# Kernel tuning notes

Measured on AMD Instinct MI355X. Metric: run time of the kernel, lower is better.

Reference implementation:

```python
import jax, jax.numpy as jnp
import numpy as np

NEG_INF = -1e30

def dwconv1(x, dw, db, pw, pb):
    # DWConv with kernel_size=1: depthwise = per-channel scale+bias, pointwise = dense linear.
    # x: [B, L, H]
    return (x * dw + db) @ pw.T + pb

def masked_softmax(logits, maskf, axis):
    # masked_softmax as in SQuAD repos: mask*logits + (1-mask)*(-1e30), then softmax over axis
    m = maskf * logits + (1.0 - maskf) * NEG_INF
    return jax.nn.softmax(m, axis=axis)

def setup_inputs() -> dict:
    key = jax.random.key(0)
    ks = jax.random.split(key, 20)
    B, L, H = 4, 4096, 1024
    s = 1.0 / np.sqrt(H)
    inp = {
        "x": jax.random.normal(ks[0], (B, L, H), dtype=jnp.float32),
        "mask": jax.random.randint(ks[1], (B, L), 0, 2, dtype=jnp.int32),
    }
    names = ["k", "q", "v", "r"]
    for i, n in enumerate(names):
        inp[n + "_dw"] = jax.random.normal(ks[2 + 4 * i], (H,), dtype=jnp.float32) * 0.1 + 1.0
        inp[n + "_db"] = jnp.zeros((H,), dtype=jnp.float32)
        inp[n + "_pw"] = jax.random.normal(ks[3 + 4 * i], (H, H), dtype=jnp.float32) * s
        inp[n + "_pb"] = jnp.zeros((H,), dtype=jnp.float32)
    return inp

def reference(x, mask, k_dw, k_db, k_pw, k_pb, q_dw, q_db, q_pw, q_pb,
              v_dw, v_db, v_pw, v_pb, r_dw, r_db, r_pw, r_pb):
    B, L, H = x.shape
    n_head = 16
    hc = H // n_head
    maskf = mask.astype(x.dtype)[:, None, None, :]  # [B,1,1,L]

    def heads(t):  # [B,L,H] -> [B,nh,hc,L]
        return t.reshape(B, L, n_head, hc).transpose(0, 2, 3, 1)

    keys = heads(dwconv1(x, k_dw, k_db, k_pw, k_pb))
    queries = heads(dwconv1(x, q_dw, q_db, q_pw, q_pb))
    values = heads(dwconv1(x, v_dw, v_db, v_pw, v_pb))

    key_sm = masked_softmax(keys, maskf, axis=3)      # softmax over L
    query_sm = masked_softmax(queries, maskf, axis=2)  # softmax over head channels

    # context = key @ value^T : [B,nh,hc,hc]
    context = jnp.einsum("bhcl,bhdl->bhcd", key_sm, values)
    # attended = context^T @ query : [B,nh,hc(value),L]
    attended = jnp.einsum("bhcd,bhcl->bhdl", context, query_sm)

    agg = attended.transpose(0, 3, 1, 2).reshape(B, L, H)  # concat heads, [B,L,H]
    # dropout is identity in eval mode
    return dwconv1(agg, r_dw, r_db, r_pw, r_pb)
```

## Files before the change

### kernel.cpp

```cpp
#include <hip/hip_runtime.h>
#include <stdint.h>

#define H 1024
#define LSEQ 4096
#define NBATCH 4
#define MT (NBATCH*LSEQ)

typedef __attribute__((ext_vector_type(8))) short bf16x8;
typedef __attribute__((ext_vector_type(4))) short s16x4;
typedef __attribute__((ext_vector_type(4))) float f32x4;
typedef __attribute__((ext_vector_type(16))) float f32x16;

static __device__ __forceinline__ unsigned short f2bf(float f){
  union { float f; unsigned u; } v; v.f = f;
  unsigned u = v.u;
  return (unsigned short)((u + 0x7FFFu + ((u >> 16) & 1u)) >> 16);
}
static __device__ __forceinline__ float bf2f(unsigned short h){
  union { unsigned u; float f; } v; v.u = ((unsigned)h) << 16;
  return v.f;
}
static __device__ __forceinline__ void g2l16(const void* g, void* l){
  __builtin_amdgcn_global_load_lds((const __attribute__((address_space(1))) void*)g,
                                   (__attribute__((address_space(3))) void*)l, 16, 0, 0);
}
static __device__ __forceinline__ f32x4 mfma16(bf16x8 a, bf16x8 b, f32x4 c){
  return __builtin_amdgcn_mfma_f32_16x16x32_bf16(a, b, c, 0, 0, 0);
}
static __device__ __forceinline__ f32x16 mfma32(bf16x8 a, bf16x8 b, f32x16 c){
  return __builtin_amdgcn_mfma_f32_32x32x16_bf16(a, b, c, 0, 0, 0);
}

struct P4 { const float* pw[4]; const float* dw[4]; const float* db[4]; const float* pb[4]; };

__global__ __launch_bounds__(256) void prepcvt(P4 a, const float* __restrict__ x,
    short* __restrict__ wb, float* __restrict__ bo, short* __restrict__ xb){
  const int bid = blockIdx.x, t = threadIdx.x;
  if (bid < 4096){
    __shared__ float red[256];
    const int p = bid >> 10, j = bid & 1023;
    const float* row = a.pw[p] + (size_t)j * H;
    const float* dwp = a.dw[p];
    const float* dbp = a.db[p];
    float acc = 0.f;
    #pragma unroll
    for (int k = 0; k < 4; ++k){
      int i = k*256 + t;
      float pv = row[i];
      wb[((size_t)p*H + j)*H + i] = (short)f2bf(pv * dwp[i]);
      acc += dbp[i] * pv;
    }
    red[t] = acc; __syncthreads();
    for (int s = 128; s > 0; s >>= 1){
      if (t < s) red[t] += red[t+s];
      __syncthreads();
    }
    if (t == 0) bo[p*H + j] = a.pb[p][j] + red[0];
  } else {
    const size_t base = ((size_t)(bid - 4096) * 4096) + (size_t)t * 16;
    #pragma unroll
    for (int h2 = 0; h2 < 2; ++h2){
      const float4* p = (const float4*)(x + base + h2*8);
      float4 u = p[0], v = p[1];
      bf16x8 o;
      o[0]=(short)f2bf(u.x); o[1]=(short)f2bf(u.y); o[2]=(short)f2bf(u.z); o[3]=(short)f2bf(u.w);
      o[4]=(short)f2bf(v.x); o[5]=(short)f2bf(v.y); o[6]=(short)f2bf(v.z); o[7]=(short)f2bf(v.w);
      *(bf16x8*)(xb + base + h2*8) = o;
    }
  }
}

template<int MODE, int NBLK>
__global__ __launch_bounds__(512, 2) void gemm8(const short* __restrict__ A,
    const short* __restrict__ WBp, const float* __restrict__ bia,
    short* __restrict__ oq, short* __restrict__ okT, short* __restrict__ ovT,
    float* __restrict__ ofin){
  __shared__ __align__(16) short lsm[2][2][256*64];

  const int nwg = NBLK * 64;
  const int cpx = nwg >> 3;
  const int bid = blockIdx.x;
  const int swz = (bid & 7) * cpx + (bid >> 3);
  const int mb = swz / NBLK, nb = swz % NBLK;
  const int m0 = mb * 256, n0 = nb * 256;

  const int tid  = threadIdx.x;
  const int lane = tid & 63;
  const int w    = tid >> 6;
  const int wm   = w >> 2, wn = w & 3;
  const int l31 = lane & 31, l1 = lane >> 5;
  const int rl = lane >> 3, sl = lane & 7;
  const int srcsw = ((sl ^ rl) << 3);

#define STAGE_A(BUF_, Q_, KB_) \
  g2l16(A + (size_t)(m0 + (Q_)*64 + w*8 + rl)*H + (KB_) + srcsw, \
        &lsm[0][BUF_][((Q_)*64 + w*8)*64])
#define STAGE_B(BUF_, Q_, KB_) \
  g2l16(WBp + (size_t)(n0 + (Q_)*64 + w*8 + rl)*H + (KB_) + srcsw, \
        &lsm[1][BUF_][((Q_)*64 + w*8)*64])
#define RD_A(dst, BUF_, MF, S) { const int row_ = wm*128 + (MF)*32 + l31; \
  dst = *(const bf16x8*)&lsm[0][BUF_][row_*64 + ((((S)*2 + l1) ^ (row_&7))<<3)]; }
#define RD_B(dst, BUF_, NF, S) { const int row_ = wn*64 + (NF)*32 + l31; \
  dst = *(const bf16x8*)&lsm[1][BUF_][row_*64 + ((((S)*2 + l1) ^ (row_&7))<<3)]; }

  f32x16 acc[4][2] = {};
  bf16x8 aF[2][4], bF[2][4];

  STAGE_B(0,0,0); STAGE_B(0,1,0); STAGE_B(0,2,0); STAGE_B(0,3,0);
  STAGE_A(0,0,0); STAGE_A(0,2,0); STAGE_A(0,1,0); STAGE_A(0,3,0);
  asm volatile("s_waitcnt vmcnt(2)" ::: "memory");
  __builtin_amdgcn_s_barrier();

  #pragma unroll 2
  for (int t = 0; t < 16; ++t){
    const int buf = t & 1, sbuf = buf ^ 1;
    const int skb = ((t < 15) ? (t + 1) : 15) << 6;

    #pragma unroll
    for (int mf = 0; mf < 2; ++mf)
      #pragma unroll
      for (int s = 0; s < 4; ++s) RD_A(aF[mf][s], buf, mf, s);
    #pragma unroll
    for (int nf = 0; nf < 2; ++nf)
      #pragma unroll
      for (int s = 0; s < 4; ++s) RD_B(bF[nf][s], buf, nf, s);
    STAGE_B(sbuf, 0, skb); STAGE_B(sbuf, 1, skb);
    STAGE_B(sbuf, 2, skb); STAGE_B(sbuf, 3, skb);
    __builtin_amdgcn_s_setprio(1);
    #pragma unroll
    for (int s = 0; s < 4; ++s)
      #pragma unroll
      for (int mf = 0; mf < 2; ++mf)
        #pragma unroll
        for (int nf = 0; nf < 2; ++nf)
          acc[mf][nf] = mfma32(aF[mf][s], bF[nf][s], acc[mf][nf]);
    __builtin_amdgcn_s_setprio(0);
    asm volatile("s_waitcnt vmcnt(4)" ::: "memory");
    __builtin_amdgcn_s_barrier();

    #pragma unroll
    for (int mf = 0; mf < 2; ++mf)
      #pragma unroll
      for (int s = 0; s < 4; ++s) RD_A(aF[mf][s], buf, 2+mf, s);
    STAGE_A(sbuf, 0, skb); STAGE_A(sbuf, 2, skb);
    STAGE_A(sbuf, 1, skb); STAGE_A(sbuf, 3, skb);
    __builtin_amdgcn_s_setprio(1);
    #pragma unroll
    for (int s = 0; s < 4; ++s)
      #pragma unroll
      for (int mf = 0; mf < 2; ++mf)
        #pragma unroll
        for (int nf = 0; nf < 2; ++nf)
          acc[2+mf][nf] = mfma32(aF[mf][s], bF[nf][s], acc[2+mf][nf]);
    __builtin_amdgcn_s_setprio(0);
    asm volatile("s_waitcnt vmcnt(2)" ::: "memory");
    __builtin_amdgcn_s_barrier();
  }
#undef STAGE_A
#undef STAGE_B
#undef RD_A
#undef RD_B

  if (MODE == 1){
    #pragma unroll
    for (int nf = 0; nf < 2; ++nf){
      const int n = n0 + wn*64 + nf*32 + l31;
      const float bv = bia[n];
      #pragma unroll
      for (int mf = 0; mf < 4; ++mf)
        #pragma unroll
        for (int g = 0; g < 4; ++g){
          const int mbse = m0 + wm*128 + mf*32 + g*8 + 4*l1;
          #pragma unroll
          for (int j = 0; j < 4; ++j)
            ofin[(size_t)(mbse+j)*H + n] = acc[mf][nf][g*4+j] + bv;
        }
    }
  } else {
    const int p = n0 >> 10;
    if (p == 1){
      #pragma unroll
      for (int nf = 0; nf < 2; ++nf){
        const int n = n0 + wn*64 + nf*32 + l31;
        const float bv = bia[n];
        const int ch = n & 1023;
        #pragma unroll
        for (int mf = 0; mf < 4; ++mf)
          #pragma unroll
          for (int g = 0; g < 4; ++g){
            const int mbse = m0 + wm*128 + mf*32 + g*8 + 4*l1;
            #pragma unroll
            for (int j = 0; j < 4; ++j)
              oq[(size_t)(mbse+j)*H + ch] = (short)f2bf(acc[mf][nf][g*4+j] + bv);
          }
      }
    } else {
      asm volatile("s_waitcnt vmcnt(0)" ::: "memory");
      __syncthreads();
      char* sC = (char*)&lsm[0][0][0];
      #pragma unroll
      for (int nf = 0; nf < 2; ++nf){
        const int cr = wn*64 + nf*32 + l31;
        const float bv = bia[n0 + cr];
        #pragma unroll
        for (int mf = 0; mf < 4; ++mf)
          #pragma unroll
          for (int g = 0; g < 4; ++g){
            const int s8 = wm*32 + mf*8 + g*2 + l1;
            s16x4 v;
            #pragma unroll
            for (int j = 0; j < 4; ++j) v[j] = (short)f2bf(acc[mf][nf][g*4+j] + bv);
            *(s16x4*)(sC + cr*512 + ((s8 ^ ((cr & 7) << 1)) << 3)) = v;
          }
      }
      __syncthreads();
      short* ot = (p == 0) ? okT : ovT;
      const int ch0 = n0 & 1023, bb = m0 >> 12, lp0 = m0 & 4095;
      const int c = lane & 31;
      #pragma unroll
      for (int it = 0; it < 16; ++it){
        const int cr = it*16 + w*2 + (lane >> 5);
        bf16x8 vv = *(bf16x8*)(sC + cr*512 + ((c ^ (cr & 7)) << 4));
        *(bf16x8*)&ot[((size_t)bb*H + ch0 + cr)*LSEQ + lp0 + c*8] = vv;
      }
    }
  }
}

__global__ __launch_bounds__(256) void ctx_k(const short* __restrict__ kT,
    const short* __restrict__ vT, const int* __restrict__ mask,
    float* __restrict__ ctxP, float* __restrict__ mloc, float* __restrict__ dloc){
  const int lc = blockIdx.x, h = blockIdx.y, b = blockIdx.z;
  __shared__ __align__(16) short lK[64*64];
  __shared__ __align__(16) short lV[64*64];
  __shared__ float sMx[64];
  __shared__ float sDenP[4][64];
  __shared__ int sMk[64];
  const int tid = threadIdx.x, lane = tid & 63, w = tid >> 6;
  const short* kb = kT + (size_t)(b*16 + h)*64*LSEQ;
  const short* vb = vT + (size_t)(b*16 + h)*64*LSEQ;
  const int l0 = lc*1024;

  int mk16[16];
  {
    const int* mp = mask + (size_t)b*LSEQ + l0;
    int4 a0 = *(const int4*)&mp[lane*8];
    int4 a1 = *(const int4*)&mp[lane*8+4];
    int4 a2 = *(const int4*)&mp[512 + lane*8];
    int4 a3 = *(const int4*)&mp[512 + lane*8+4];
    mk16[0]=a0.x; mk16[1]=a0.y; mk16[2]=a0.z; mk16[3]=a0.w;
    mk16[4]=a1.x; mk16[5]=a1.y; mk16[6]=a1.z; mk16[7]=a1.w;
    mk16[8]=a2.x; mk16[9]=a2.y; mk16[10]=a2.z; mk16[11]=a2.w;
    mk16[12]=a3.x; mk16[13]=a3.y; mk16[14]=a3.z; mk16[15]=a3.w;
  }
  for (int c2 = 0; c2 < 16; ++c2){
    const int ch = w*16 + c2;
    const short* rp = kb + (size_t)ch*LSEQ + l0;
    bf16x8 v0 = *(const bf16x8*)&rp[lane*8];
    bf16x8 v1 = *(const bf16x8*)&rp[512 + lane*8];
    float mm = -1e30f;
    #pragma unroll
    for (int e = 0; e < 8; ++e) if (mk16[e])   mm = fmaxf(mm, bf2f((unsigned short)v0[e]));
    #pragma unroll
    for (int e = 0; e < 8; ++e) if (mk16[8+e]) mm = fmaxf(mm, bf2f((unsigned short)v1[e]));
    #pragma unroll
    for (int off = 32; off >= 1; off >>= 1) mm = fmaxf(mm, __shfl_xor(mm, off));
    if (lane == 0) sMx[ch] = mm;
  }

  f32x4 acc[4] = {};
  float dsum = 0.f;
  const int sl = lane & 7, rl = lane >> 3;
  const int lsw = ((sl ^ rl) << 3);
  __syncthreads();
  for (int kc = 0; kc < 16; ++kc){
    __syncthreads();
    const int lb = l0 + kc*64;
    #pragma unroll
    for (int c = 0; c < 2; ++c){
      const int r = (w*2+c)*8 + rl;
      g2l16(kb + (size_t)r*LSEQ + lb + lsw, &lK[(w*2+c)*512]);
      g2l16(vb + (size_t)r*LSEQ + lb + lsw, &lV[(w*2+c)*512]);
    }
    if (tid < 64) sMk[tid] = mask[(size_t)b*LSEQ + lb + tid];
    __syncthreads();
    {
      const int row = lane;
      const float mxr = sMx[row];
      #pragma unroll
      for (int k2 = 0; k2 < 2; ++k2){
        const int slog = w*2 + k2;
        const int sp = slog ^ (row & 7);
        bf16x8 v = *(bf16x8*)&lK[row*64 + (sp<<3)];
        bf16x8 o;
        #pragma unroll
        for (int e=0;e<8;++e){
          const float f = bf2f((unsigned short)v[e]);
          const float we = sMk[slog*8+e] ? __expf(f - mxr) : 0.0f;
          dsum += we;
          o[e] = (short)f2bf(we);
        }
        *(bf16x8*)&lK[row*64 + (sp<<3)] = o;
      }
    }
    __syncthreads();
    const int q4 = lane >> 4, r16 = lane & 15;
    #pragma unroll
    for (int kk = 0; kk < 2; ++kk){
      const int slog = kk*4 + q4;
      const int rowA = w*16 + r16;
      bf16x8 a = *(bf16x8*)&lK[rowA*64 + ((slog ^ (rowA & 7))<<3)];
      #pragma unroll
      for (int ni = 0; ni < 4; ++ni){
        const int rowB = ni*16 + r16;
        bf16x8 bv = *(bf16x8*)&lV[rowB*64 + ((slog ^ (rowB & 7))<<3)];
        acc[ni] = mfma16(a, bv, acc[ni]);
      }
    }
  }
  const int q4 = lane >> 4, r16 = lane & 15;
  float* op = ctxP + (((size_t)(b*16 + h)*4 + lc) << 12);
  #pragma unroll
  for (int ni=0;ni<4;++ni){
    const int d = ni*16 + r16;
    #pragma unroll
    for (int j=0;j<4;++j){
      const int c = w*16 + q4*4 + j;
      op[c*64 + d] = acc[ni][j];
    }
  }
  sDenP[w][lane] = dsum;
  __syncthreads();
  if (tid < 64){
    const int idx = (((b*16 + h)*4 + lc) << 6) + tid;
    mloc[idx] = sMx[tid];
    dloc[idx] = sDenP[0][tid] + sDenP[1][tid] + sDenP[2][tid] + sDenP[3][tid];
  }
}

__global__ __launch_bounds__(256) void attd_k(const short* __restrict__ qb,
    const float* __restrict__ ctxP, const float* __restrict__ mloc,
    const float* __restrict__ dloc, const int* __restrict__ mask,
    short* __restrict__ agg){
  const int lcb = blockIdx.x, h = blockIdx.y, b = blockIdx.z;
  __shared__ __align__(16) short lQ[64*64];
  __shared__ __align__(16) short lCt[64*64];
  __shared__ float sSc[4][64];
  const int tid = threadIdx.x, lane = tid & 63, w = tid >> 6;
  if (tid < 64){
    const int base = ((b*16 + h) << 8) + tid;
    float m0 = mloc[base], m1 = mloc[base+64], m2 = mloc[base+128], m3 = mloc[base+192];
    float mg = fmaxf(fmaxf(m0,m1), fmaxf(m2,m3));
    float e0 = __expf(m0-mg), e1 = __expf(m1-mg), e2 = __expf(m2-mg), e3 = __expf(m3-mg);
    float den = e0*dloc[base] + e1*dloc[base+64] + e2*dloc[base+128] + e3*dloc[base+192];
    float inv = 1.0f / fmaxf(den, 1e-30f);
    sSc[0][tid] = e0*inv; sSc[1][tid] = e1*inv; sSc[2][tid] = e2*inv; sSc[3][tid] = e3*inv;
  }
  __syncthreads();
  {
    const int d = lane, g = w;
    const float* base = ctxP + ((size_t)(b*16 + h)*4 << 12);
    #pragma unroll
    for (int i=0;i<16;++i){
      const int c = g*16 + i;
      const float s = base[c*64+d]*sSc[0][c] + base[4096+c*64+d]*sSc[1][c]
                    + base[8192+c*64+d]*sSc[2][c] + base[12288+c*64+d]*sSc[3][c];
      lCt[d*64 + ((((c>>3) ^ (d&7))<<3) | (c&7))] = (short)f2bf(s);
    }
  }
  const int l0g = b*LSEQ + lcb*1024;
  const int sl = lane & 7, rl = lane >> 3;
  const int lsw = ((sl ^ rl) << 3);
  for (int sc = 0; sc < 16; ++sc){
    __syncthreads();
    #pragma unroll
    for (int c = 0; c < 2; ++c){
      const int r = (w*2+c)*8 + rl;
      g2l16(qb + (size_t)(l0g + sc*64 + r)*H + h*64 + lsw, &lQ[(w*2+c)*512]);
    }
    __syncthreads();
    {
      const int row = w*16 + (lane & 15);
      const int q4 = lane >> 4;
      const int mk = mask[(size_t)b*LSEQ + lcb*1024 + sc*64 + row];
      float vals[16];
      float mxv = -3e38f;
      #pragma unroll
      for (int k2=0;k2<2;++k2){
        const int slog = q4*2 + k2;
        const int sp = slog ^ (row & 7);
        bf16x8 v = *(bf16x8*)&lQ[row*64 + (sp<<3)];
        #pragma unroll
        for (int e=0;e<8;++e){
          const float f = bf2f((unsigned short)v[e]);
          vals[k2*8+e] = f;
          mxv = fmaxf(mxv, f);
        }
      }
      mxv = fmaxf(mxv, __shfl_xor(mxv, 16));
      mxv = fmaxf(mxv, __shfl_xor(mxv, 32));
      float s = 0.f;
      #pragma unroll
      for (int e=0;e<16;++e){ vals[e] = __expf(vals[e]-mxv); s += vals[e]; }
      s += __shfl_xor(s, 16);
      s += __shfl_xor(s, 32);
      const float inv = 1.0f / s;
      #pragma unroll
      for (int k2=0;k2<2;++k2){
        const int slog = q4*2 + k2;
        const int sp = slog ^ (row & 7);
        bf16x8 o;
        #pragma unroll
        for (int e=0;e<8;++e)
          o[e] = (short)f2bf(mk ? vals[k2*8+e]*inv : 0.015625f);
        *(bf16x8*)&lQ[row*64 + (sp<<3)] = o;
      }
    }
    __syncthreads();
    f32x4 acc[4] = {};
    const int q4 = lane >> 4, r16 = lane & 15;
    #pragma unroll
    for (int kk=0;kk<2;++kk){
      const int slog = kk*4 + q4;
      const int rowA = w*16 + r16;
      bf16x8 a = *(bf16x8*)&lQ[rowA*64 + ((slog ^ (rowA&7))<<3)];
      #pragma unroll
      for (int ni=0;ni<4;++ni){
        const int rowB = ni*16 + r16;
        bf16x8 bv = *(bf16x8*)&lCt[rowB*64 + ((slog ^ (rowB&7))<<3)];
        acc[ni] = mfma16(a, bv, acc[ni]);
      }
    }
    #pragma unroll
    for (int ni=0;ni<4;++ni){
      const int d = ni*16 + r16;
      #pragma unroll
      for (int j=0;j<4;++j){
        const int lrow = w*16 + q4*4 + j;
        agg[(size_t)(l0g + sc*64 + lrow)*H + h*64 + d] = (short)f2bf(acc[ni][j]);
      }
    }
  }
}

extern "C" void kernel_launch(void* const* d_in, const int* in_sizes, int n_in,
                              void* d_out, int out_size, void* d_ws, size_t ws_size,
                              hipStream_t stream){
  (void)in_sizes; (void)n_in; (void)out_size; (void)ws_size;
  const float* x    = (const float*)d_in[0];
  const int*   mask = (const int*)d_in[1];
  P4 prm;
  for (int p2 = 0; p2 < 4; ++p2){
    prm.dw[p2] = (const float*)d_in[2 + 4*p2];
    prm.db[p2] = (const float*)d_in[3 + 4*p2];
    prm.pw[p2] = (const float*)d_in[4 + 4*p2];
    prm.pb[p2] = (const float*)d_in[5 + 4*p2];
  }
  char* ws = (char*)d_ws;
  short* WB   = (short*)(ws);
  float* BIAS = (float*)(ws + ((size_t)8<<20));
  float* MLOC = (float*)(ws + ((size_t)8<<20) + (1<<16));
  float* DLOC = (float*)(ws + ((size_t)8<<20) + (2<<16));
  short* XB   = (short*)(ws + ((size_t)9<<20));
  short* QB   = (short*)(ws + ((size_t)41<<20));
  short* KT   = (short*)(ws + ((size_t)73<<20));
  short* VT   = (short*)(ws + ((size_t)105<<20));
  float* CTXP = (float*)(ws + ((size_t)137<<20));
  short* AGG  = XB;

  prepcvt<<<8192, 256, 0, stream>>>(prm, x, WB, BIAS, XB);
  gemm8<0,12><<<768, 512, 0, stream>>>(XB, WB, BIAS, QB, KT, VT, nullptr);
  ctx_k<<<dim3(4,16,4), 256, 0, stream>>>(KT, VT, mask, CTXP, MLOC, DLOC);
  attd_k<<<dim3(4,16,4), 256, 0, stream>>>(QB, CTXP, MLOC, DLOC, mask, AGG);
  gemm8<1,4><<<256, 512, 0, stream>>>(AGG, WB + (size_t)3*H*H, BIAS + 3*1024,
                                      nullptr, nullptr, nullptr, (float*)d_out);
}
```

Measured before the change: 242.2 us.

## Switch GEMM to 16x16 MFMA tiles and double warps in attention kernels

The GEMM inner loop moves from 32x32x16 MFMA to 16x16x32 MFMA fragments, with new LDS read patterns and epilogue indexing. The ctx and attended kernels now launch 512 threads, split into two groups that each handle half of the sequence chunk. Partial context accumulators from the two groups are combined through shared memory. The goal is to raise parallelism in the small 256-block attention kernels and change the GEMM's MFMA issue pattern, at the cost of more LDS use and a different accumulator register layout.

```diff
diff --git a/kernel.cpp b/kernel.cpp
--- a/kernel.cpp
+++ b/kernel.cpp
@@ -9,7 +9,6 @@
 typedef __attribute__((ext_vector_type(8))) short bf16x8;
 typedef __attribute__((ext_vector_type(4))) short s16x4;
 typedef __attribute__((ext_vector_type(4))) float f32x4;
-typedef __attribute__((ext_vector_type(16))) float f32x16;
 
 static __device__ __forceinline__ unsigned short f2bf(float f){
   union { float f; unsigned u; } v; v.f = f;
@@ -26,9 +25,6 @@
 }
 static __device__ __forceinline__ f32x4 mfma16(bf16x8 a, bf16x8 b, f32x4 c){
   return __builtin_amdgcn_mfma_f32_16x16x32_bf16(a, b, c, 0, 0, 0);
-}
-static __device__ __forceinline__ f32x16 mfma32(bf16x8 a, bf16x8 b, f32x16 c){
-  return __builtin_amdgcn_mfma_f32_32x32x16_bf16(a, b, c, 0, 0, 0);
 }
 
 struct P4 { const float* pw[4]; const float* dw[4]; const float* db[4]; const float* pb[4]; };
@@ -88,7 +84,7 @@
   const int lane = tid & 63;
   const int w    = tid >> 6;
   const int wm   = w >> 2, wn = w & 3;
-  const int l31 = lane & 31, l1 = lane >> 5;
+  const int q4 = lane >> 4, r16 = lane & 15;
   const int rl = lane >> 3, sl = lane & 7;
   const int srcsw = ((sl ^ rl) << 3);
 
@@ -98,13 +94,13 @@
 #define STAGE_B(BUF_, Q_, KB_) \
   g2l16(WBp + (size_t)(n0 + (Q_)*64 + w*8 + rl)*H + (KB_) + srcsw, \
         &lsm[1][BUF_][((Q_)*64 + w*8)*64])
-#define RD_A(dst, BUF_, MF, S) { const int row_ = wm*128 + (MF)*32 + l31; \
-  dst = *(const bf16x8*)&lsm[0][BUF_][row_*64 + ((((S)*2 + l1) ^ (row_&7))<<3)]; }
-#define RD_B(dst, BUF_, NF, S) { const int row_ = wn*64 + (NF)*32 + l31; \
-  dst = *(const bf16x8*)&lsm[1][BUF_][row_*64 + ((((S)*2 + l1) ^ (row_&7))<<3)]; }
-
-  f32x16 acc[4][2] = {};
-  bf16x8 aF[2][4], bF[2][4];
+#define RD_A(dst, BUF_, MI8, KK) { const int row_ = wm*128 + (MI8)*16 + r16; \
+  dst = *(const bf16x8*)&lsm[0][BUF_][row_*64 + ((((KK)*4+q4) ^ (row_&7))<<3)]; }
+#define RD_B(dst, BUF_, NI4, KK) { const int row_ = wn*64 + (NI4)*16 + r16; \
+  dst = *(const bf16x8*)&lsm[1][BUF_][row_*64 + ((((KK)*4+q4) ^ (row_&7))<<3)]; }
+
+  f32x4 acc[8][4] = {};
+  bf16x8 aF[4][2], bFa[2][2], bFb[2][2];
 
   STAGE_B(0,0,0); STAGE_B(0,1,0); STAGE_B(0,2,0); STAGE_B(0,3,0);
   STAGE_A(0,0,0); STAGE_A(0,2,0); STAGE_A(0,1,0); STAGE_A(0,3,0);
@@ -117,41 +113,45 @@
     const int skb = ((t < 15) ? (t + 1) : 15) << 6;
 
     #pragma unroll
-    for (int mf = 0; mf < 2; ++mf)
-      #pragma unroll
-      for (int s = 0; s < 4; ++s) RD_A(aF[mf][s], buf, mf, s);
-    #pragma unroll
-    for (int nf = 0; nf < 2; ++nf)
-      #pragma unroll
-      for (int s = 0; s < 4; ++s) RD_B(bF[nf][s], buf, nf, s);
+    for (int mi = 0; mi < 4; ++mi){ RD_A(aF[mi][0], buf, mi, 0); RD_A(aF[mi][1], buf, mi, 1); }
+    #pragma unroll
+    for (int ni = 0; ni < 2; ++ni){ RD_B(bFa[ni][0], buf, ni, 0); RD_B(bFa[ni][1], buf, ni, 1); }
+    #pragma unroll
+    for (int ni = 0; ni < 2; ++ni){ RD_B(bFb[ni][0], buf, 2+ni, 0); RD_B(bFb[ni][1], buf, 2+ni, 1); }
     STAGE_B(sbuf, 0, skb); STAGE_B(sbuf, 1, skb);
     STAGE_B(sbuf, 2, skb); STAGE_B(sbuf, 3, skb);
     __builtin_amdgcn_s_setprio(1);
     #pragma unroll
-    for (int s = 0; s < 4; ++s)
-      #pragma unroll
-      for (int mf = 0; mf < 2; ++mf)
-        #pragma unroll
-        for (int nf = 0; nf < 2; ++nf)
-          acc[mf][nf] = mfma32(aF[mf][s], bF[nf][s], acc[mf][nf]);
+    for (int kk = 0; kk < 2; ++kk)
+      #pragma unroll
+      for (int mi = 0; mi < 4; ++mi){
+        #pragma unroll
+        for (int ni = 0; ni < 2; ++ni)
+          acc[mi][ni] = mfma16(aF[mi][kk], bFa[ni][kk], acc[mi][ni]);
+        #pragma unroll
+        for (int ni = 0; ni < 2; ++ni)
+          acc[mi][2+ni] = mfma16(aF[mi][kk], bFb[ni][kk], acc[mi][2+ni]);
+      }
     __builtin_amdgcn_s_setprio(0);
     asm volatile("s_waitcnt vmcnt(4)" ::: "memory");
     __builtin_amdgcn_s_barrier();
 
     #pragma unroll
-    for (int mf = 0; mf < 2; ++mf)
-      #pragma unroll
-      for (int s = 0; s < 4; ++s) RD_A(aF[mf][s], buf, 2+mf, s);
+    for (int mi = 0; mi < 4; ++mi){ RD_A(aF[mi][0], buf, 4+mi, 0); RD_A(aF[mi][1], buf, 4+mi, 1); }
     STAGE_A(sbuf, 0, skb); STAGE_A(sbuf, 2, skb);
     STAGE_A(sbuf, 1, skb); STAGE_A(sbuf, 3, skb);
     __builtin_amdgcn_s_setprio(1);
     #pragma unroll
-    for (int s = 0; s < 4; ++s)
-      #pragma unroll
-      for (int mf = 0; mf < 2; ++mf)
-        #pragma unroll
-        for (int nf = 0; nf < 2; ++nf)
-          acc[2+mf][nf] = mfma32(aF[mf][s], bF[nf][s], acc[2+mf][nf]);
+    for (int kk = 0; kk < 2; ++kk)
+      #pragma unroll
+      for (int mi = 0; mi < 4; ++mi){
+        #pragma unroll
+        for (int ni = 0; ni < 2; ++ni)
+          acc[4+mi][ni] = mfma16(aF[mi][kk], bFa[ni][kk], acc[4+mi][ni]);
+        #pragma unroll
+        for (int ni = 0; ni < 2; ++ni)
+          acc[4+mi][2+ni] = mfma16(aF[mi][kk], bFb[ni][kk], acc[4+mi][2+ni]);
+      }
     __builtin_amdgcn_s_setprio(0);
     asm volatile("s_waitcnt vmcnt(2)" ::: "memory");
     __builtin_amdgcn_s_barrier();
@@ -163,55 +163,49 @@
 
   if (MODE == 1){
     #pragma unroll
-    for (int nf = 0; nf < 2; ++nf){
-      const int n = n0 + wn*64 + nf*32 + l31;
+    for (int ni4 = 0; ni4 < 4; ++ni4){
+      const int n = n0 + wn*64 + ni4*16 + r16;
       const float bv = bia[n];
       #pragma unroll
-      for (int mf = 0; mf < 4; ++mf)
-        #pragma unroll
-        for (int g = 0; g < 4; ++g){
-          const int mbse = m0 + wm*128 + mf*32 + g*8 + 4*l1;
-          #pragma unroll
-          for (int j = 0; j < 4; ++j)
-            ofin[(size_t)(mbse+j)*H + n] = acc[mf][nf][g*4+j] + bv;
-        }
+      for (int mi8 = 0; mi8 < 8; ++mi8){
+        const int mbse = m0 + wm*128 + mi8*16 + q4*4;
+        #pragma unroll
+        for (int j = 0; j < 4; ++j)
+          ofin[(size_t)(mbse+j)*H + n] = acc[mi8][ni4][j] + bv;
+      }
     }
   } else {
     const int p = n0 >> 10;
     if (p == 1){
       #pragma unroll
-      for (int nf = 0; nf < 2; ++nf){
-        const int n = n0 + wn*64 + nf*32 + l31;
+      for (int ni4 = 0; ni4 < 4; ++ni4){
+        const int n = n0 + wn*64 + ni4*16 + r16;
         const float bv = bia[n];
         const int ch = n & 1023;
         #pragma unroll
-        for (int mf = 0; mf < 4; ++mf)
+        for (int mi8 = 0; mi8 < 8; ++mi8){
+          const int mbse = m0 + wm*128 + mi8*16 + q4*4;
           #pragma unroll
-          for (int g = 0; g < 4; ++g){
-            const int mbse = m0 + wm*128 + mf*32 + g*8 + 4*l1;
-            #pragma unroll
-            for (int j = 0; j < 4; ++j)
-              oq[(size_t)(mbse+j)*H + ch] = (short)f2bf(acc[mf][nf][g*4+j] + bv);
-          }
+          for (int j = 0; j < 4; ++j)
+            oq[(size_t)(mbse+j)*H + ch] = (short)f2bf(acc[mi8][ni4][j] + bv);
+        }
       }
     } else {
       asm volatile("s_waitcnt vmcnt(0)" ::: "memory");
       __syncthreads();
       char* sC = (char*)&lsm[0][0][0];
       #pragma unroll
-      for (int nf = 0; nf < 2; ++nf){
-        const int cr = wn*64 + nf*32 + l31;
+      for (int ni4 = 0; ni4 < 4; ++ni4){
+        const int cr = wn*64 + ni4*16 + r16;
         const float bv = bia[n0 + cr];
         #pragma unroll
-        for (int mf = 0; mf < 4; ++mf)
+        for (int mi8 = 0; mi8 < 8; ++mi8){
+          const int s8 = wm*32 + mi8*4 + q4;
+          s16x4 v;
           #pragma unroll
-          for (int g = 0; g < 4; ++g){
-            const int s8 = wm*32 + mf*8 + g*2 + l1;
-            s16x4 v;
-            #pragma unroll
-            for (int j = 0; j < 4; ++j) v[j] = (short)f2bf(acc[mf][nf][g*4+j] + bv);
-            *(s16x4*)(sC + cr*512 + ((s8 ^ ((cr & 7) << 1)) << 3)) = v;
-          }
+          for (int j = 0; j < 4; ++j) v[j] = (short)f2bf(acc[mi8][ni4][j] + bv);
+          *(s16x4*)(sC + cr*512 + ((s8 ^ ((cr & 7) << 1)) << 3)) = v;
+        }
       }
       __syncthreads();
       short* ot = (p == 0) ? okT : ovT;
@@ -227,16 +221,18 @@
   }
 }
 
-__global__ __launch_bounds__(256) void ctx_k(const short* __restrict__ kT,
+__global__ __launch_bounds__(512) void ctx_k(const short* __restrict__ kT,
     const short* __restrict__ vT, const int* __restrict__ mask,
     float* __restrict__ ctxP, float* __restrict__ mloc, float* __restrict__ dloc){
   const int lc = blockIdx.x, h = blockIdx.y, b = blockIdx.z;
-  __shared__ __align__(16) short lK[64*64];
-  __shared__ __align__(16) short lV[64*64];
+  __shared__ __align__(16) short lK[2][64*64];
+  __shared__ __align__(16) short lV[2][64*64];
   __shared__ float sMx[64];
-  __shared__ float sDenP[4][64];
-  __shared__ int sMk[64];
+  __shared__ float sDenP[8][64];
+  __shared__ int sMkG[2][64];
+  __shared__ float sAcc[64][65];
   const int tid = threadIdx.x, lane = tid & 63, w = tid >> 6;
+  const int grp = w >> 2, wg = w & 3, tig = tid & 255;
   const short* kb = kT + (size_t)(b*16 + h)*64*LSEQ;
   const short* vb = vT + (size_t)(b*16 + h)*64*LSEQ;
   const int l0 = lc*1024;
@@ -253,8 +249,9 @@
     mk16[8]=a2.x; mk16[9]=a2.y; mk16[10]=a2.z; mk16[11]=a2.w;
     mk16[12]=a3.x; mk16[13]=a3.y; mk16[14]=a3.z; mk16[15]=a3.w;
   }
-  for (int c2 = 0; c2 < 16; ++c2){
-    const int ch = w*16 + c2;
+  #pragma unroll
+  for (int c2 = 0; c2 < 8; ++c2){
+    const int ch = w*8 + c2;
     const short* rp = kb + (size_t)ch*LSEQ + l0;
     bf16x8 v0 = *(const bf16x8*)&rp[lane*8];
     bf16x8 v1 = *(const bf16x8*)&rp[512 + lane*8];
@@ -273,34 +270,35 @@
   const int sl = lane & 7, rl = lane >> 3;
   const int lsw = ((sl ^ rl) << 3);
   __syncthreads();
-  for (int kc = 0; kc < 16; ++kc){
+  for (int kc2 = 0; kc2 < 8; ++kc2){
+    const int kc = kc2*2 + grp;
     __syncthreads();
     const int lb = l0 + kc*64;
     #pragma unroll
     for (int c = 0; c < 2; ++c){
-      const int r = (w*2+c)*8 + rl;
-      g2l16(kb + (size_t)r*LSEQ + lb + lsw, &lK[(w*2+c)*512]);
-      g2l16(vb + (size_t)r*LSEQ + lb + lsw, &lV[(w*2+c)*512]);
-    }
-    if (tid < 64) sMk[tid] = mask[(size_t)b*LSEQ + lb + tid];
+      const int r = (wg*2+c)*8 + rl;
+      g2l16(kb + (size_t)r*LSEQ + lb + lsw, &lK[grp][(wg*2+c)*512]);
+      g2l16(vb + (size_t)r*LSEQ + lb + lsw, &lV[grp][(wg*2+c)*512]);
+    }
+    if (tig < 64) sMkG[grp][tig] = mask[(size_t)b*LSEQ + lb + tig];
     __syncthreads();
     {
       const int row = lane;
       const float mxr = sMx[row];
       #pragma unroll
       for (int k2 = 0; k2 < 2; ++k2){
-        const int slog = w*2 + k2;
+        const int slog = wg*2 + k2;
         const int sp = slog ^ (row & 7);
-        bf16x8 v = *(bf16x8*)&lK[row*64 + (sp<<3)];
+        bf16x8 v = *(bf16x8*)&lK[grp][row*64 + (sp<<3)];
         bf16x8 o;
         #pragma unroll
         for (int e=0;e<8;++e){
           const float f = bf2f((unsigned short)v[e]);
-          const float we = sMk[slog*8+e] ? __expf(f - mxr) : 0.0f;
+          const float we = sMkG[grp][slog*8+e] ? __expf(f - mxr) : 0.0f;
           dsum += we;
           o[e] = (short)f2bf(we);
         }
-        *(bf16x8*)&lK[row*64 + (sp<<3)] = o;
+        *(bf16x8*)&lK[grp][row*64 + (sp<<3)] = o;
       }
     }
     __syncthreads();
@@ -308,45 +306,60 @@
     #pragma unroll
     for (int kk = 0; kk < 2; ++kk){
       const int slog = kk*4 + q4;
-      const int rowA = w*16 + r16;
-      bf16x8 a = *(bf16x8*)&lK[rowA*64 + ((slog ^ (rowA & 7))<<3)];
+      const int rowA = wg*16 + r16;
+      bf16x8 a = *(bf16x8*)&lK[grp][rowA*64 + ((slog ^ (rowA & 7))<<3)];
       #pragma unroll
       for (int ni = 0; ni < 4; ++ni){
         const int rowB = ni*16 + r16;
-        bf16x8 bv = *(bf16x8*)&lV[rowB*64 + ((slog ^ (rowB & 7))<<3)];
+        bf16x8 bv = *(bf16x8*)&lV[grp][rowB*64 + ((slog ^ (rowB & 7))<<3)];
         acc[ni] = mfma16(a, bv, acc[ni]);
       }
     }
   }
   const int q4 = lane >> 4, r16 = lane & 15;
-  float* op = ctxP + (((size_t)(b*16 + h)*4 + lc) << 12);
-  #pragma unroll
-  for (int ni=0;ni<4;++ni){
-    const int d = ni*16 + r16;
-    #pragma unroll
-    for (int j=0;j<4;++j){
-      const int c = w*16 + q4*4 + j;
-      op[c*64 + d] = acc[ni][j];
-    }
-  }
   sDenP[w][lane] = dsum;
+  if (grp == 0){
+    #pragma unroll
+    for (int ni=0;ni<4;++ni){
+      const int d = ni*16 + r16;
+      #pragma unroll
+      for (int j=0;j<4;++j)
+        sAcc[wg*16 + q4*4 + j][d] = acc[ni][j];
+    }
+  }
   __syncthreads();
+  if (grp == 1){
+    float* op = ctxP + (((size_t)(b*16 + h)*4 + lc) << 12);
+    #pragma unroll
+    for (int ni=0;ni<4;++ni){
+      const int d = ni*16 + r16;
+      #pragma unroll
+      for (int j=0;j<4;++j){
+        const int c = wg*16 + q4*4 + j;
+        op[c*64 + d] = acc[ni][j] + sAcc[c][d];
+      }
+    }
+  }
   if (tid < 64){
     const int idx = (((b*16 + h)*4 + lc) << 6) + tid;
     mloc[idx] = sMx[tid];
-    dloc[idx] = sDenP[0][tid] + sDenP[1][tid] + sDenP[2][tid] + sDenP[3][tid];
-  }
-}
-
-__global__ __launch_bounds__(256) void attd_k(const short* __restrict__ qb,
+    float dv = 0.f;
+    #pragma unroll
+    for (int ww = 0; ww < 8; ++ww) dv += sDenP[ww][tid];
+    dloc[idx] = dv;
+  }
+}
+
+__global__ __launch_bounds__(512) void attd_k(const short* __restrict__ qb,
     const float* __restrict__ ctxP, const float* __restrict__ mloc,
     const float* __restrict__ dloc, const int* __restrict__ mask,
     short* __restrict__ agg){
   const int lcb = blockIdx.x, h = blockIdx.y, b = blockIdx.z;
-  __shared__ __align__(16) short lQ[64*64];
+  __shared__ __align__(16) short lQ[2][64*64];
   __shared__ __align__(16) short lCt[64*64];
   __shared__ float sSc[4][64];
   const int tid = threadIdx.x, lane = tid & 63, w = tid >> 6;
+  const int grp = w >> 2, wg = w & 3;
   if (tid < 64){
     const int base = ((b*16 + h) << 8) + tid;
     float m0 = mloc[base], m1 = mloc[base+64], m2 = mloc[base+128], m3 = mloc[base+192];
@@ -358,38 +371,38 @@
   }
   __syncthreads();
   {
-    const int d = lane, g = w;
+    const int d = lane;
     const float* base = ctxP + ((size_t)(b*16 + h)*4 << 12);
     #pragma unroll
-    for (int i=0;i<16;++i){
-      const int c = g*16 + i;
+    for (int i=0;i<8;++i){
+      const int c = w*8 + i;
       const float s = base[c*64+d]*sSc[0][c] + base[4096+c*64+d]*sSc[1][c]
                     + base[8192+c*64+d]*sSc[2][c] + base[12288+c*64+d]*sSc[3][c];
       lCt[d*64 + ((((c>>3) ^ (d&7))<<3) | (c&7))] = (short)f2bf(s);
     }
   }
-  const int l0g = b*LSEQ + lcb*1024;
+  const int l0g = b*LSEQ + lcb*1024 + grp*512;
   const int sl = lane & 7, rl = lane >> 3;
   const int lsw = ((sl ^ rl) << 3);
-  for (int sc = 0; sc < 16; ++sc){
+  for (int sc = 0; sc < 8; ++sc){
     __syncthreads();
     #pragma unroll
     for (int c = 0; c < 2; ++c){
-      const int r = (w*2+c)*8 + rl;
-      g2l16(qb + (size_t)(l0g + sc*64 + r)*H + h*64 + lsw, &lQ[(w*2+c)*512]);
+      const int r = (wg*2+c)*8 + rl;
+      g2l16(qb + (size_t)(l0g + sc*64 + r)*H + h*64 + lsw, &lQ[grp][(wg*2+c)*512]);
     }
     __syncthreads();
     {
-      const int row = w*16 + (lane & 15);
+      const int row = wg*16 + (lane & 15);
       const int q4 = lane >> 4;
-      const int mk = mask[(size_t)b*LSEQ + lcb*1024 + sc*64 + row];
+      const int mk = mask[(size_t)l0g + sc*64 + row];
       float vals[16];
       float mxv = -3e38f;
       #pragma unroll
       for (int k2=0;k2<2;++k2){
         const int slog = q4*2 + k2;
         const int sp = slog ^ (row & 7);
-        bf16x8 v = *(bf16x8*)&lQ[row*64 + (sp<<3)];
+        bf16x8 v = *(bf16x8*)&lQ[grp][row*64 + (sp<<3)];
         #pragma unroll
         for (int e=0;e<8;++e){
           const float f = bf2f((unsigned short)v[e]);
@@ -413,7 +426,7 @@
         #pragma unroll
         for (int e=0;e<8;++e)
           o[e] = (short)f2bf(mk ? vals[k2*8+e]*inv : 0.015625f);
-        *(bf16x8*)&lQ[row*64 + (sp<<3)] = o;
+        *(bf16x8*)&lQ[grp][row*64 + (sp<<3)] = o;
       }
     }
     __syncthreads();
@@ -422,8 +435,8 @@
     #pragma unroll
     for (int kk=0;kk<2;++kk){
       const int slog = kk*4 + q4;
-      const int rowA = w*16 + r16;
-      bf16x8 a = *(bf16x8*)&lQ[rowA*64 + ((slog ^ (rowA&7))<<3)];
+      const int rowA = wg*16 + r16;
+      bf16x8 a = *(bf16x8*)&lQ[grp][rowA*64 + ((slog ^ (rowA&7))<<3)];
       #pragma unroll
       for (int ni=0;ni<4;++ni){
         const int rowB = ni*16 + r16;
@@ -436,7 +449,7 @@
       const int d = ni*16 + r16;
       #pragma unroll
       for (int j=0;j<4;++j){
-        const int lrow = w*16 + q4*4 + j;
+        const int lrow = wg*16 + q4*4 + j;
         agg[(size_t)(l0g + sc*64 + lrow)*H + h*64 + d] = (short)f2bf(acc[ni][j]);
       }
     }
@@ -470,8 +483,8 @@
 
   prepcvt<<<8192, 256, 0, stream>>>(prm, x, WB, BIAS, XB);
   gemm8<0,12><<<768, 512, 0, stream>>>(XB, WB, BIAS, QB, KT, VT, nullptr);
-  ctx_k<<<dim3(4,16,4), 256, 0, stream>>>(KT, VT, mask, CTXP, MLOC, DLOC);
-  attd_k<<<dim3(4,16,4), 256, 0, stream>>>(QB, CTXP, MLOC, DLOC, mask, AGG);
+  ctx_k<<<dim3(4,16,4), 512, 0, stream>>>(KT, VT, mask, CTXP, MLOC, DLOC);
+  attd_k<<<dim3(4,16,4), 512, 0, stream>>>(QB, CTXP, MLOC, DLOC, mask, AGG);
   gemm8<1,4><<<256, 512, 0, stream>>>(AGG, WB + (size_t)3*H*H, BIAS + 3*1024,
                                       nullptr, nullptr, nullptr, (float*)d_out);
 }
```

New measurement: 209.6 us. 1.16x faster.
